# Performance work log

Hardware: AMD Instinct MI355X
Metric: run time of the kernel (lower is better)

Reference implementation:

```python
import jax, jax.numpy as jnp
import numpy as np

N_NODES = 100000
N_EDGES = 1600000
IN_CH = 128


def _sage_conv(x, src, dst, Wl, b, Wr, n_nodes):
    # PyG SAGEConv (aggr='mean', root_weight=True):
    #   out_i = lin_l(mean_{j->i} x_j) + lin_r(x_i)
    msg = x[src]                                             # [E, F]
    agg = jax.ops.segment_sum(msg, dst, num_segments=n_nodes)  # [N, F]
    deg = jax.ops.segment_sum(jnp.ones((src.shape[0],), x.dtype), dst,
                              num_segments=n_nodes)          # [N]
    mean = agg / jnp.maximum(deg, 1.0)[:, None]
    return mean @ Wl + b + x @ Wr


def setup_inputs() -> dict:
    key = jax.random.key(0)
    ks = jax.random.split(key, 10)
    x = jax.random.normal(ks[0], (N_NODES, IN_CH), dtype=jnp.float32)
    edge_index = jax.random.randint(ks[1], (2, N_EDGES), 0, N_NODES, dtype=jnp.int64)
    s = 0.05
    return {
        "x": x,
        "edge_index": edge_index,
        "W1l": jax.random.normal(ks[2], (IN_CH, 32), dtype=jnp.float32) * s,
        "b1": jax.random.normal(ks[3], (32,), dtype=jnp.float32) * s,
        "W1r": jax.random.normal(ks[4], (IN_CH, 32), dtype=jnp.float32) * s,
        "W2l": jax.random.normal(ks[5], (32, 16), dtype=jnp.float32) * s,
        "b2": jax.random.normal(ks[6], (16,), dtype=jnp.float32) * s,
        "W2r": jax.random.normal(ks[7], (32, 16), dtype=jnp.float32) * s,
        "Wfc": jax.random.normal(ks[8], (16, 2), dtype=jnp.float32) * s,
        "bfc": jax.random.normal(ks[9], (2,), dtype=jnp.float32) * s,
    }


def reference(x, edge_index, W1l, b1, W1r, W2l, b2, W2r, Wfc, bfc):
    src, dst = edge_index[0], edge_index[1]
    n = x.shape[0]
    h = jax.nn.relu(_sage_conv(x, src, dst, W1l, b1, W1r, n))   # [N, 32]
    h = jax.nn.relu(_sage_conv(h, src, dst, W2l, b2, W2r, n))   # [N, 16]
    return h @ Wfc + bfc                                        # [N, 2]
```

## Files before the change

kernel.cpp:

```cpp
#include <hip/hip_runtime.h>

#define TPB 256
#define BK_SHIFT 7
#define BK_SIZE 128
#define NBK_MAX 784
#define CAP 2816
#define SC_EPB 8192
#define GEMM_BLKS 1024

typedef __attribute__((ext_vector_type(8))) short bf16x8;
typedef __attribute__((ext_vector_type(4))) float f32x4;
typedef __attribute__((ext_vector_type(2))) float f32x2;
typedef __attribute__((ext_vector_type(4))) unsigned short u16x4;

__device__ __forceinline__ unsigned short f2bf(float f) {
    unsigned u = __float_as_uint(f);
    unsigned r = (u + 0x7FFFu + ((u >> 16) & 1u)) >> 16;
    return (unsigned short)r;
}
__device__ __forceinline__ float bf2f(unsigned short b) {
    return __uint_as_float((unsigned)b << 16);
}
__device__ __forceinline__ void acc4(f32x4& a, u16x4 v) {
    a.x += bf2f(v.x); a.y += bf2f(v.y); a.z += bf2f(v.z); a.w += bf2f(v.w);
}

__global__ __launch_bounds__(256) void build_and_gemm1(
    const int* __restrict__ src, const int* __restrict__ dst,
    int* __restrict__ gfill, int* __restrict__ pk, int E, int NBK, int NSC,
    const float* __restrict__ A,
    const float* __restrict__ Wl,
    const float* __restrict__ Wr,
    const float* __restrict__ b,
    unsigned short* __restrict__ Yb,
    float* __restrict__ C,
    int N)
{
    __shared__ int lcnt[NBK_MAX];
    __shared__ int lbase[NBK_MAX];
    __shared__ int lrank[NBK_MAX];

    if ((int)blockIdx.x < NSC) {
        const int t = threadIdx.x;
        const int e0 = blockIdx.x * SC_EPB;

        for (int i = t; i < NBK; i += 256) { lcnt[i] = 0; lrank[i] = 0; }
        __syncthreads();

        #pragma unroll
        for (int k = 0; k < SC_EPB / 1024; ++k) {
            int e = e0 + k * 1024 + t * 4;
            if (e < E) {
                int4 d = *(const int4*)&dst[e];
                atomicAdd(&lcnt[d.x >> BK_SHIFT], 1);
                atomicAdd(&lcnt[d.y >> BK_SHIFT], 1);
                atomicAdd(&lcnt[d.z >> BK_SHIFT], 1);
                atomicAdd(&lcnt[d.w >> BK_SHIFT], 1);
            }
        }
        __syncthreads();

        for (int i = t; i < NBK; i += 256) {
            int c = lcnt[i];
            if (c) lbase[i] = atomicAdd(&gfill[i], c);
        }
        __syncthreads();

        #pragma unroll
        for (int k = 0; k < SC_EPB / 1024; ++k) {
            int e = e0 + k * 1024 + t * 4;
            if (e < E) {
                int4 d = *(const int4*)&dst[e];
                int4 s = *(const int4*)&src[e];
                {
                    int bb = d.x >> BK_SHIFT;
                    int pos = lbase[bb] + atomicAdd(&lrank[bb], 1);
                    if (pos < CAP) pk[(size_t)bb * CAP + pos] =
                        (s.x << BK_SHIFT) | (d.x & (BK_SIZE - 1));
                }
                {
                    int bb = d.y >> BK_SHIFT;
                    int pos = lbase[bb] + atomicAdd(&lrank[bb], 1);
                    if (pos < CAP) pk[(size_t)bb * CAP + pos] =
                        (s.y << BK_SHIFT) | (d.y & (BK_SIZE - 1));
                }
                {
                    int bb = d.z >> BK_SHIFT;
                    int pos = lbase[bb] + atomicAdd(&lrank[bb], 1);
                    if (pos < CAP) pk[(size_t)bb * CAP + pos] =
                        (s.z << BK_SHIFT) | (d.z & (BK_SIZE - 1));
                }
                {
                    int bb = d.w >> BK_SHIFT;
                    int pos = lbase[bb] + atomicAdd(&lrank[bb], 1);
                    if (pos < CAP) pk[(size_t)bb * CAP + pos] =
                        (s.w << BK_SHIFT) | (d.w & (BK_SIZE - 1));
                }
            }
        }
        return;
    }

    const int lane = threadIdx.x & 63;
    const int m    = lane & 15;
    const int quad = lane >> 4;
    const int wave   = (blockIdx.x - NSC) * (blockDim.x >> 6) + (threadIdx.x >> 6);
    const int nwaves = GEMM_BLKS * (blockDim.x >> 6);
    const int ntiles = (N + 15) >> 4;

    bf16x8 Bf[4][4];
    #pragma unroll
    for (int kc = 0; kc < 4; ++kc) {
        #pragma unroll
        for (int jt = 0; jt < 4; ++jt) {
            const float* W = (jt < 2) ? Wl : Wr;
            const int col = (jt & 1) * 16 + m;
            #pragma unroll
            for (int j = 0; j < 8; ++j) {
                int k = kc * 32 + quad * 8 + j;
                Bf[kc][jt][j] = (short)f2bf(W[k * 32 + col]);
            }
        }
    }

    const float bias0 = b[m];
    const float bias1 = b[16 + m];

    for (int tile = wave; tile < ntiles; tile += nwaves) {
        const int node0 = tile * 16;
        const int gn = node0 + m;
        const bool okA = gn < N;
        const float* rowp = A + (size_t)gn * 128;

        bf16x8 Af[4];
        #pragma unroll
        for (int kc = 0; kc < 4; ++kc) {
            f32x4 v0 = {0.f, 0.f, 0.f, 0.f};
            f32x4 v1 = {0.f, 0.f, 0.f, 0.f};
            if (okA) {
                v0 = __builtin_nontemporal_load((const f32x4*)&rowp[kc * 32 + quad * 8]);
                v1 = __builtin_nontemporal_load((const f32x4*)&rowp[kc * 32 + quad * 8 + 4]);
            }
            Af[kc][0] = (short)f2bf(v0.x); Af[kc][1] = (short)f2bf(v0.y);
            Af[kc][2] = (short)f2bf(v0.z); Af[kc][3] = (short)f2bf(v0.w);
            Af[kc][4] = (short)f2bf(v1.x); Af[kc][5] = (short)f2bf(v1.y);
            Af[kc][6] = (short)f2bf(v1.z); Af[kc][7] = (short)f2bf(v1.w);
        }

        f32x4 acc[4] = {{0.f,0.f,0.f,0.f},{0.f,0.f,0.f,0.f},
                        {0.f,0.f,0.f,0.f},{0.f,0.f,0.f,0.f}};
        #pragma unroll
        for (int kc = 0; kc < 4; ++kc) {
            #pragma unroll
            for (int jt = 0; jt < 4; ++jt)
                acc[jt] = __builtin_amdgcn_mfma_f32_16x16x32_bf16(
                    Af[kc], Bf[kc][jt], acc[jt], 0, 0, 0);
        }

        const int nodeBase = node0 + quad * 4;
        #pragma unroll
        for (int reg = 0; reg < 4; ++reg) {
            const int node = nodeBase + reg;
            if (node < N) {
                Yb[(size_t)node * 32 + m]      = f2bf(acc[0][reg]);
                Yb[(size_t)node * 32 + 16 + m] = f2bf(acc[1][reg]);
                C [(size_t)node * 32 + m]      = acc[2][reg] + bias0;
                C [(size_t)node * 32 + 16 + m] = acc[3][reg] + bias1;
            }
        }
    }
}

__global__ __launch_bounds__(256) void gather_gemm2(
    const int* __restrict__ gfill, const int* __restrict__ pk,
    const unsigned short* __restrict__ Yb,
    const float* __restrict__ c1,
    const float* __restrict__ W2l, const float* __restrict__ W2r,
    const float* __restrict__ b2,
    unsigned short* __restrict__ y2b, float* __restrict__ c2, int N)
{
    __shared__ int lcnt[BK_SIZE];
    __shared__ int soff[BK_SIZE];
    __shared__ int wcur[BK_SIZE];
    __shared__ int sidx[CAP];

    const int t = threadIdx.x;
    const int b = blockIdx.x;
    const size_t base = (size_t)b * CAP;
    const int cnt  = min(gfill[b], CAP);
    const int node0 = b * BK_SIZE;

    if (t < BK_SIZE) lcnt[t] = 0;
    __syncthreads();

    for (int j = t; j < cnt; j += 256)
        atomicAdd(&lcnt[pk[base + j] & (BK_SIZE - 1)], 1);
    __syncthreads();

    int v = (t < BK_SIZE) ? lcnt[t] : 0;
    if (t < BK_SIZE) soff[t] = v;
    __syncthreads();
    for (int off = 1; off < BK_SIZE; off <<= 1) {
        int u = (t < BK_SIZE && t >= off) ? soff[t - off] : 0;
        __syncthreads();
        if (t < BK_SIZE) soff[t] += u;
        __syncthreads();
    }
    if (t < BK_SIZE) wcur[t] = soff[t] - v;
    __syncthreads();

    for (int j = t; j < cnt; j += 256) {
        int pv = pk[base + j];
        int d  = pv & (BK_SIZE - 1);
        int pos = atomicAdd(&wcur[d], 1);
        sidx[pos] = pv >> BK_SHIFT;
    }
    __syncthreads();

    const int q = t & 7;
    #pragma unroll
    for (int pass = 0; pass < 4; ++pass) {
        const int nl = pass * 32 + (t >> 3);
        const int node = node0 + nl;
        const bool active = node < N;
        float h[4] = {0.f, 0.f, 0.f, 0.f};
        if (active) {
            const int deg = lcnt[nl];
            const int en  = soff[nl];
            const int st  = en - deg;
            const float w = 1.0f / fmaxf((float)deg, 1.0f);

            f32x4 a0 = {0.f,0.f,0.f,0.f};
            f32x4 a1 = {0.f,0.f,0.f,0.f};
            f32x4 a2 = {0.f,0.f,0.f,0.f};
            f32x4 a3 = {0.f,0.f,0.f,0.f};
            int j = st;
            for (; j + 3 < en; j += 4) {
                int s0 = sidx[j], s1 = sidx[j+1], s2 = sidx[j+2], s3 = sidx[j+3];
                u16x4 v0 = *(const u16x4*)&Yb[(size_t)s0 * 32 + q * 4];
                u16x4 v1 = *(const u16x4*)&Yb[(size_t)s1 * 32 + q * 4];
                u16x4 v2 = *(const u16x4*)&Yb[(size_t)s2 * 32 + q * 4];
                u16x4 v3 = *(const u16x4*)&Yb[(size_t)s3 * 32 + q * 4];
                acc4(a0, v0); acc4(a1, v1); acc4(a2, v2); acc4(a3, v3);
            }
            for (; j < en; ++j) {
                u16x4 vv = *(const u16x4*)&Yb[(size_t)sidx[j] * 32 + q * 4];
                acc4(a0, vv);
            }
            f32x4 acc;
            acc.x = (a0.x + a1.x) + (a2.x + a3.x);
            acc.y = (a0.y + a1.y) + (a2.y + a3.y);
            acc.z = (a0.z + a1.z) + (a2.z + a3.z);
            acc.w = (a0.w + a1.w) + (a2.w + a3.w);

            f32x4 c = __builtin_nontemporal_load((const f32x4*)&c1[(size_t)node * 32 + q * 4]);
            h[0] = fmaxf(c.x + acc.x * w, 0.f);
            h[1] = fmaxf(c.y + acc.y * w, 0.f);
            h[2] = fmaxf(c.z + acc.z * w, 0.f);
            h[3] = fmaxf(c.w + acc.w * w, 0.f);
        }

        const int  j0  = q * 4;
        const bool isY = (j0 < 16);
        const int  jj  = isY ? j0 : (j0 - 16);
        const float* Wb = isY ? W2l : W2r;

        float o0 = 0.f, o1 = 0.f, o2 = 0.f, o3 = 0.f;
        #pragma unroll
        for (int k = 0; k < 32; ++k) {
            float hk = __shfl(h[k & 3], k >> 2, 8);
            f32x4 wv = *(const f32x4*)&Wb[k * 16 + jj];
            o0 += hk * wv.x; o1 += hk * wv.y; o2 += hk * wv.z; o3 += hk * wv.w;
        }

        if (active) {
            if (isY) {
                u16x4 r;
                r.x = f2bf(o0); r.y = f2bf(o1); r.z = f2bf(o2); r.w = f2bf(o3);
                *(u16x4*)&y2b[(size_t)node * 16 + jj] = r;
            } else {
                f32x4 bb = *(const f32x4*)&b2[jj];
                f32x4 ov = {o0 + bb.x, o1 + bb.y, o2 + bb.z, o3 + bb.w};
                __builtin_nontemporal_store(ov, (f32x4*)&c2[(size_t)node * 16 + jj]);
            }
        }
    }
}

__global__ __launch_bounds__(256) void gather_final(
    const int* __restrict__ gfill, const int* __restrict__ pk,
    const unsigned short* __restrict__ Yb,
    const float* __restrict__ c2,
    const float* __restrict__ Wfc,
    const float* __restrict__ bfc,
    float* __restrict__ out, int N)
{
    __shared__ int lcnt[BK_SIZE];
    __shared__ int soff[BK_SIZE];
    __shared__ int wcur[BK_SIZE];
    __shared__ int sidx[CAP];

    const int t = threadIdx.x;
    const int b = blockIdx.x;
    const size_t base = (size_t)b * CAP;
    const int cnt  = min(gfill[b], CAP);
    const int node0 = b * BK_SIZE;

    if (t < BK_SIZE) lcnt[t] = 0;
    __syncthreads();

    for (int j = t; j < cnt; j += 256)
        atomicAdd(&lcnt[pk[base + j] & (BK_SIZE - 1)], 1);
    __syncthreads();

    int v = (t < BK_SIZE) ? lcnt[t] : 0;
    if (t < BK_SIZE) soff[t] = v;
    __syncthreads();
    for (int off = 1; off < BK_SIZE; off <<= 1) {
        int u = (t < BK_SIZE && t >= off) ? soff[t - off] : 0;
        __syncthreads();
        if (t < BK_SIZE) soff[t] += u;
        __syncthreads();
    }
    if (t < BK_SIZE) wcur[t] = soff[t] - v;
    __syncthreads();

    for (int j = t; j < cnt; j += 256) {
        int pv = pk[base + j];
        int d  = pv & (BK_SIZE - 1);
        int pos = atomicAdd(&wcur[d], 1);
        sidx[pos] = pv >> BK_SHIFT;
    }
    __syncthreads();

    const int q = t & 3;
    #pragma unroll
    for (int pass = 0; pass < 2; ++pass) {
        const int nl = pass * 64 + (t >> 2);
        const int node = node0 + nl;
        if (node < N) {
            const int deg = lcnt[nl];
            const int en  = soff[nl];
            const int st  = en - deg;
            const float w = 1.0f / fmaxf((float)deg, 1.0f);

            f32x4 a0 = {0.f,0.f,0.f,0.f};
            f32x4 a1 = {0.f,0.f,0.f,0.f};
            f32x4 a2 = {0.f,0.f,0.f,0.f};
            f32x4 a3 = {0.f,0.f,0.f,0.f};
            int j = st;
            for (; j + 3 < en; j += 4) {
                int s0 = sidx[j], s1 = sidx[j+1], s2 = sidx[j+2], s3 = sidx[j+3];
                u16x4 v0 = *(const u16x4*)&Yb[(size_t)s0 * 16 + q * 4];
                u16x4 v1 = *(const u16x4*)&Yb[(size_t)s1 * 16 + q * 4];
                u16x4 v2 = *(const u16x4*)&Yb[(size_t)s2 * 16 + q * 4];
                u16x4 v3 = *(const u16x4*)&Yb[(size_t)s3 * 16 + q * 4];
                acc4(a0, v0); acc4(a1, v1); acc4(a2, v2); acc4(a3, v3);
            }
            for (; j < en; ++j) {
                u16x4 vv = *(const u16x4*)&Yb[(size_t)sidx[j] * 16 + q * 4];
                acc4(a0, vv);
            }
            f32x4 acc;
            acc.x = (a0.x + a1.x) + (a2.x + a3.x);
            acc.y = (a0.y + a1.y) + (a2.y + a3.y);
            acc.z = (a0.z + a1.z) + (a2.z + a3.z);
            acc.w = (a0.w + a1.w) + (a2.w + a3.w);

            f32x4 c = __builtin_nontemporal_load((const f32x4*)&c2[(size_t)node * 16 + q * 4]);
            float h0 = fmaxf(c.x + acc.x * w, 0.f);
            float h1 = fmaxf(c.y + acc.y * w, 0.f);
            float h2 = fmaxf(c.z + acc.z * w, 0.f);
            float h3 = fmaxf(c.w + acc.w * w, 0.f);

            const float* Wq = &Wfc[q * 8];
            float o0 = h0 * Wq[0] + h1 * Wq[2] + h2 * Wq[4] + h3 * Wq[6];
            float o1 = h0 * Wq[1] + h1 * Wq[3] + h2 * Wq[5] + h3 * Wq[7];

            o0 += __shfl_xor(o0, 1); o0 += __shfl_xor(o0, 2);
            o1 += __shfl_xor(o1, 1); o1 += __shfl_xor(o1, 2);

            if (q == 0) {
                f32x2 ov = {o0 + bfc[0], o1 + bfc[1]};
                __builtin_nontemporal_store(ov, (f32x2*)&out[(size_t)node * 2]);
            }
        } else {
            float z = 0.f;
            z += __shfl_xor(z, 1); z += __shfl_xor(z, 2);
        }
    }
}

extern "C" void kernel_launch(void* const* d_in, const int* in_sizes, int n_in,
                              void* d_out, int out_size, void* d_ws, size_t ws_size,
                              hipStream_t stream)
{
    const float* x   = (const float*)d_in[0];
    const int*   ei  = (const int*)d_in[1];
    const float* W1l = (const float*)d_in[2];
    const float* b1  = (const float*)d_in[3];
    const float* W1r = (const float*)d_in[4];
    const float* W2l = (const float*)d_in[5];
    const float* b2  = (const float*)d_in[6];
    const float* W2r = (const float*)d_in[7];
    const float* Wfc = (const float*)d_in[8];
    const float* bfc = (const float*)d_in[9];
    float* out = (float*)d_out;

    const int N = in_sizes[0] / 128;
    const int E = in_sizes[1] / 2;
    const int* src = ei;
    const int* dst = ei + E;

    const int NBK = (N + BK_SIZE - 1) / BK_SIZE;
    const int NSC = (E + SC_EPB - 1) / SC_EPB;

    int*   gfill = (int*)d_ws;
    int*   pk    = gfill + NBK_MAX;
    unsigned short* y1b = (unsigned short*)(pk + (size_t)NBK_MAX * CAP);
    float* c1          = (float*)(y1b + (size_t)N * 32);
    unsigned short* y2b = (unsigned short*)(c1 + (size_t)N * 32);
    float* c2          = (float*)(y2b + (size_t)N * 16);

    hipMemsetAsync(gfill, 0, (size_t)NBK_MAX * sizeof(int), stream);
    build_and_gemm1<<<NSC + GEMM_BLKS, TPB, 0, stream>>>(
        src, dst, gfill, pk, E, NBK, NSC,
        x, W1l, W1r, b1, y1b, c1, N);

    gather_gemm2<<<NBK, TPB, 0, stream>>>(
        gfill, pk, y1b, c1, W2l, W2r, b2, y2b, c2, N);

    gather_final<<<NBK, TPB, 0, stream>>>(
        gfill, pk, y2b, c2, Wfc, bfc, out, N);
}
```

Before: 201.9 us.

## Fuse all three stages into one persistent kernel with grid barriers

Merges edge bucketing plus GEMM1, gather plus GEMM2, and the final gather into one kernel launched with NBK blocks, separated by atomic-counter grid barriers. GEMM1 tiles are handed out through a global atomic work counter in batches instead of a fixed stride over dedicated blocks. The aim is to remove two kernel launches and their tails, and to let scatter blocks pick up GEMM work after they finish. In exchange the grid barrier relies on all NBK blocks (about 782) being co-resident, which risks deadlock, and it adds barrier spin cost.

```diff
diff --git a/kernel.cpp b/kernel.cpp
--- a/kernel.cpp
+++ b/kernel.cpp
@@ -6,7 +6,7 @@
 #define NBK_MAX 784
 #define CAP 2816
 #define SC_EPB 8192
-#define GEMM_BLKS 1024
+#define TILE_BATCH 2
 
 typedef __attribute__((ext_vector_type(8))) short bf16x8;
 typedef __attribute__((ext_vector_type(4))) float f32x4;
@@ -25,24 +25,46 @@
     a.x += bf2f(v.x); a.y += bf2f(v.y); a.z += bf2f(v.z); a.w += bf2f(v.w);
 }
 
-__global__ __launch_bounds__(256) void build_and_gemm1(
+__device__ __forceinline__ void grid_barrier(int* bar, int nblk) {
+    __syncthreads();
+    if (threadIdx.x == 0) {
+        __threadfence();
+        atomicAdd(bar, 1);
+        while (atomicAdd(bar, 0) < nblk)
+            __builtin_amdgcn_s_sleep(2);
+        __threadfence();
+    }
+    __syncthreads();
+}
+
+__global__ __launch_bounds__(256, 4) void fused_all(
     const int* __restrict__ src, const int* __restrict__ dst,
-    int* __restrict__ gfill, int* __restrict__ pk, int E, int NBK, int NSC,
+    int* __restrict__ gfill, int* __restrict__ tcur, int* __restrict__ bar,
+    int* __restrict__ pk,
+    int E, int NBK, int NSC,
     const float* __restrict__ A,
-    const float* __restrict__ Wl,
-    const float* __restrict__ Wr,
-    const float* __restrict__ b,
-    unsigned short* __restrict__ Yb,
-    float* __restrict__ C,
-    int N)
+    const float* __restrict__ W1l, const float* __restrict__ W1r,
+    const float* __restrict__ b1,
+    unsigned short* __restrict__ y1b,
+    float* __restrict__ c1,
+    const float* __restrict__ W2l, const float* __restrict__ W2r,
+    const float* __restrict__ b2,
+    unsigned short* __restrict__ y2b,
+    float* __restrict__ c2,
+    const float* __restrict__ Wfc, const float* __restrict__ bfc,
+    float* __restrict__ out, int N)
 {
-    __shared__ int lcnt[NBK_MAX];
-    __shared__ int lbase[NBK_MAX];
-    __shared__ int lrank[NBK_MAX];
-
-    if ((int)blockIdx.x < NSC) {
-        const int t = threadIdx.x;
-        const int e0 = blockIdx.x * SC_EPB;
+    __shared__ int smem[3200];
+
+    const int t    = threadIdx.x;
+    const int bid  = blockIdx.x;
+    const int lane = t & 63;
+
+    if (bid < NSC) {
+        int* lcnt  = smem;
+        int* lbase = smem + 784;
+        int* lrank = smem + 1568;
+        const int e0 = bid * SC_EPB;
 
         for (int i = t; i < NBK; i += 256) { lcnt[i] = 0; lrank[i] = 0; }
         __syncthreads();
@@ -98,295 +120,290 @@
                 }
             }
         }
-        return;
     }
 
-    const int lane = threadIdx.x & 63;
-    const int m    = lane & 15;
-    const int quad = lane >> 4;
-    const int wave   = (blockIdx.x - NSC) * (blockDim.x >> 6) + (threadIdx.x >> 6);
-    const int nwaves = GEMM_BLKS * (blockDim.x >> 6);
-    const int ntiles = (N + 15) >> 4;
-
-    bf16x8 Bf[4][4];
-    #pragma unroll
-    for (int kc = 0; kc < 4; ++kc) {
-        #pragma unroll
-        for (int jt = 0; jt < 4; ++jt) {
-            const float* W = (jt < 2) ? Wl : Wr;
-            const int col = (jt & 1) * 16 + m;
-            #pragma unroll
-            for (int j = 0; j < 8; ++j) {
-                int k = kc * 32 + quad * 8 + j;
-                Bf[kc][jt][j] = (short)f2bf(W[k * 32 + col]);
-            }
-        }
-    }
-
-    const float bias0 = b[m];
-    const float bias1 = b[16 + m];
-
-    for (int tile = wave; tile < ntiles; tile += nwaves) {
-        const int node0 = tile * 16;
-        const int gn = node0 + m;
-        const bool okA = gn < N;
-        const float* rowp = A + (size_t)gn * 128;
-
-        bf16x8 Af[4];
-        #pragma unroll
-        for (int kc = 0; kc < 4; ++kc) {
-            f32x4 v0 = {0.f, 0.f, 0.f, 0.f};
-            f32x4 v1 = {0.f, 0.f, 0.f, 0.f};
-            if (okA) {
-                v0 = __builtin_nontemporal_load((const f32x4*)&rowp[kc * 32 + quad * 8]);
-                v1 = __builtin_nontemporal_load((const f32x4*)&rowp[kc * 32 + quad * 8 + 4]);
-            }
-            Af[kc][0] = (short)f2bf(v0.x); Af[kc][1] = (short)f2bf(v0.y);
-            Af[kc][2] = (short)f2bf(v0.z); Af[kc][3] = (short)f2bf(v0.w);
-            Af[kc][4] = (short)f2bf(v1.x); Af[kc][5] = (short)f2bf(v1.y);
-            Af[kc][6] = (short)f2bf(v1.z); Af[kc][7] = (short)f2bf(v1.w);
-        }
-
-        f32x4 acc[4] = {{0.f,0.f,0.f,0.f},{0.f,0.f,0.f,0.f},
-                        {0.f,0.f,0.f,0.f},{0.f,0.f,0.f,0.f}};
+    {
+        const int m    = lane & 15;
+        const int quad = lane >> 4;
+        const int ntiles = (N + 15) >> 4;
+
+        bf16x8 Bf[4][4];
         #pragma unroll
         for (int kc = 0; kc < 4; ++kc) {
             #pragma unroll
-            for (int jt = 0; jt < 4; ++jt)
-                acc[jt] = __builtin_amdgcn_mfma_f32_16x16x32_bf16(
-                    Af[kc], Bf[kc][jt], acc[jt], 0, 0, 0);
-        }
-
-        const int nodeBase = node0 + quad * 4;
+            for (int jt = 0; jt < 4; ++jt) {
+                const float* W = (jt < 2) ? W1l : W1r;
+                const int col = (jt & 1) * 16 + m;
+                #pragma unroll
+                for (int j = 0; j < 8; ++j) {
+                    int k = kc * 32 + quad * 8 + j;
+                    Bf[kc][jt][j] = (short)f2bf(W[k * 32 + col]);
+                }
+            }
+        }
+
+        const float bias0 = b1[m];
+        const float bias1 = b1[16 + m];
+
+        for (;;) {
+            int t0 = 0;
+            if (lane == 0) t0 = atomicAdd(tcur, TILE_BATCH);
+            t0 = __shfl(t0, 0, 64);
+            if (t0 >= ntiles) break;
+
+            for (int it = 0; it < TILE_BATCH; ++it) {
+                const int tile = t0 + it;
+                if (tile >= ntiles) break;
+                const int node0 = tile * 16;
+                const int gn = node0 + m;
+                const bool okA = gn < N;
+                const float* rowp = A + (size_t)gn * 128;
+
+                bf16x8 Af[4];
+                #pragma unroll
+                for (int kc = 0; kc < 4; ++kc) {
+                    f32x4 v0 = {0.f, 0.f, 0.f, 0.f};
+                    f32x4 v1 = {0.f, 0.f, 0.f, 0.f};
+                    if (okA) {
+                        v0 = __builtin_nontemporal_load((const f32x4*)&rowp[kc * 32 + quad * 8]);
+                        v1 = __builtin_nontemporal_load((const f32x4*)&rowp[kc * 32 + quad * 8 + 4]);
+                    }
+                    Af[kc][0] = (short)f2bf(v0.x); Af[kc][1] = (short)f2bf(v0.y);
+                    Af[kc][2] = (short)f2bf(v0.z); Af[kc][3] = (short)f2bf(v0.w);
+                    Af[kc][4] = (short)f2bf(v1.x); Af[kc][5] = (short)f2bf(v1.y);
+                    Af[kc][6] = (short)f2bf(v1.z); Af[kc][7] = (short)f2bf(v1.w);
+                }
+
+                f32x4 acc[4] = {{0.f,0.f,0.f,0.f},{0.f,0.f,0.f,0.f},
+                                {0.f,0.f,0.f,0.f},{0.f,0.f,0.f,0.f}};
+                #pragma unroll
+                for (int kc = 0; kc < 4; ++kc) {
+                    #pragma unroll
+                    for (int jt = 0; jt < 4; ++jt)
+                        acc[jt] = __builtin_amdgcn_mfma_f32_16x16x32_bf16(
+                            Af[kc], Bf[kc][jt], acc[jt], 0, 0, 0);
+                }
+
+                const int nodeBase = node0 + quad * 4;
+                #pragma unroll
+                for (int reg = 0; reg < 4; ++reg) {
+                    const int node = nodeBase + reg;
+                    if (node < N) {
+                        y1b[(size_t)node * 32 + m]      = f2bf(acc[0][reg]);
+                        y1b[(size_t)node * 32 + 16 + m] = f2bf(acc[1][reg]);
+                        c1 [(size_t)node * 32 + m]      = acc[2][reg] + bias0;
+                        c1 [(size_t)node * 32 + 16 + m] = acc[3][reg] + bias1;
+                    }
+                }
+            }
+        }
+    }
+
+    grid_barrier(&bar[0], NBK);
+
+    {
+        int* lcnt = smem;
+        int* soff = smem + 128;
+        int* wcur = smem + 256;
+        int* sidx = smem + 384;
+
+        const int b = bid;
+        const size_t base = (size_t)b * CAP;
+        const int cnt  = min(gfill[b], CAP);
+        const int node0 = b * BK_SIZE;
+
+        if (t < BK_SIZE) lcnt[t] = 0;
+        __syncthreads();
+
+        for (int j = t; j < cnt; j += 256)
+            atomicAdd(&lcnt[pk[base + j] & (BK_SIZE - 1)], 1);
+        __syncthreads();
+
+        int v = (t < BK_SIZE) ? lcnt[t] : 0;
+        if (t < BK_SIZE) soff[t] = v;
+        __syncthreads();
+        for (int off = 1; off < BK_SIZE; off <<= 1) {
+            int u = (t < BK_SIZE && t >= off) ? soff[t - off] : 0;
+            __syncthreads();
+            if (t < BK_SIZE) soff[t] += u;
+            __syncthreads();
+        }
+        if (t < BK_SIZE) wcur[t] = soff[t] - v;
+        __syncthreads();
+
+        for (int j = t; j < cnt; j += 256) {
+            int pv = pk[base + j];
+            int d  = pv & (BK_SIZE - 1);
+            int pos = atomicAdd(&wcur[d], 1);
+            sidx[pos] = pv >> BK_SHIFT;
+        }
+        __syncthreads();
+
+        const int q = t & 7;
         #pragma unroll
-        for (int reg = 0; reg < 4; ++reg) {
-            const int node = nodeBase + reg;
+        for (int pass = 0; pass < 4; ++pass) {
+            const int nl = pass * 32 + (t >> 3);
+            const int node = node0 + nl;
+            const bool active = node < N;
+            float h[4] = {0.f, 0.f, 0.f, 0.f};
+            if (active) {
+                const int deg = lcnt[nl];
+                const int en  = soff[nl];
+                const int st  = en - deg;
+                const float w = 1.0f / fmaxf((float)deg, 1.0f);
+
+                f32x4 a0 = {0.f,0.f,0.f,0.f};
+                f32x4 a1 = {0.f,0.f,0.f,0.f};
+                f32x4 a2 = {0.f,0.f,0.f,0.f};
+                f32x4 a3 = {0.f,0.f,0.f,0.f};
+                int j = st;
+                for (; j + 3 < en; j += 4) {
+                    int s0 = sidx[j], s1 = sidx[j+1], s2 = sidx[j+2], s3 = sidx[j+3];
+                    u16x4 v0 = *(const u16x4*)&y1b[(size_t)s0 * 32 + q * 4];
+                    u16x4 v1 = *(const u16x4*)&y1b[(size_t)s1 * 32 + q * 4];
+                    u16x4 v2 = *(const u16x4*)&y1b[(size_t)s2 * 32 + q * 4];
+                    u16x4 v3 = *(const u16x4*)&y1b[(size_t)s3 * 32 + q * 4];
+                    acc4(a0, v0); acc4(a1, v1); acc4(a2, v2); acc4(a3, v3);
+                }
+                for (; j < en; ++j) {
+                    u16x4 vv = *(const u16x4*)&y1b[(size_t)sidx[j] * 32 + q * 4];
+                    acc4(a0, vv);
+                }
+                f32x4 acc;
+                acc.x = (a0.x + a1.x) + (a2.x + a3.x);
+                acc.y = (a0.y + a1.y) + (a2.y + a3.y);
+                acc.z = (a0.z + a1.z) + (a2.z + a3.z);
+                acc.w = (a0.w + a1.w) + (a2.w + a3.w);
+
+                f32x4 c = *(const f32x4*)&c1[(size_t)node * 32 + q * 4];
+                h[0] = fmaxf(c.x + acc.x * w, 0.f);
+                h[1] = fmaxf(c.y + acc.y * w, 0.f);
+                h[2] = fmaxf(c.z + acc.z * w, 0.f);
+                h[3] = fmaxf(c.w + acc.w * w, 0.f);
+            }
+
+            const int  j0  = q * 4;
+            const bool isY = (j0 < 16);
+            const int  jj  = isY ? j0 : (j0 - 16);
+            const float* Wb = isY ? W2l : W2r;
+
+            float o0 = 0.f, o1 = 0.f, o2 = 0.f, o3 = 0.f;
+            #pragma unroll
+            for (int k = 0; k < 32; ++k) {
+                float hk = __shfl(h[k & 3], k >> 2, 8);
+                f32x4 wv = *(const f32x4*)&Wb[k * 16 + jj];
+                o0 += hk * wv.x; o1 += hk * wv.y; o2 += hk * wv.z; o3 += hk * wv.w;
+            }
+
+            if (active) {
+                if (isY) {
+                    u16x4 r;
+                    r.x = f2bf(o0); r.y = f2bf(o1); r.z = f2bf(o2); r.w = f2bf(o3);
+                    *(u16x4*)&y2b[(size_t)node * 16 + jj] = r;
+                } else {
+                    f32x4 bb = *(const f32x4*)&b2[jj];
+                    f32x4 ov = {o0 + bb.x, o1 + bb.y, o2 + bb.z, o3 + bb.w};
+                    *(f32x4*)&c2[(size_t)node * 16 + jj] = ov;
+                }
+            }
+        }
+    }
+
+    grid_barrier(&bar[16], NBK);
+
+    {
+        int* lcnt = smem;
+        int* soff = smem + 128;
+        int* wcur = smem + 256;
+        int* sidx = smem + 384;
+
+        const int b = bid;
+        const size_t base = (size_t)b * CAP;
+        const int cnt  = min(gfill[b], CAP);
+        const int node0 = b * BK_SIZE;
+
+        if (t < BK_SIZE) lcnt[t] = 0;
+        __syncthreads();
+
+        for (int j = t; j < cnt; j += 256)
+            atomicAdd(&lcnt[pk[base + j] & (BK_SIZE - 1)], 1);
+        __syncthreads();
+
+        int v = (t < BK_SIZE) ? lcnt[t] : 0;
+        if (t < BK_SIZE) soff[t] = v;
+        __syncthreads();
+        for (int off = 1; off < BK_SIZE; off <<= 1) {
+            int u = (t < BK_SIZE && t >= off) ? soff[t - off] : 0;
+            __syncthreads();
+            if (t < BK_SIZE) soff[t] += u;
+            __syncthreads();
+        }
+        if (t < BK_SIZE) wcur[t] = soff[t] - v;
+        __syncthreads();
+
+        for (int j = t; j < cnt; j += 256) {
+            int pv = pk[base + j];
+            int d  = pv & (BK_SIZE - 1);
+            int pos = atomicAdd(&wcur[d], 1);
+            sidx[pos] = pv >> BK_SHIFT;
+        }
+        __syncthreads();
+
+        const int q = t & 3;
+        #pragma unroll
+        for (int pass = 0; pass < 2; ++pass) {
+            const int nl = pass * 64 + (t >> 2);
+            const int node = node0 + nl;
             if (node < N) {
-                Yb[(size_t)node * 32 + m]      = f2bf(acc[0][reg]);
-                Yb[(size_t)node * 32 + 16 + m] = f2bf(acc[1][reg]);
-                C [(size_t)node * 32 + m]      = acc[2][reg] + bias0;
-                C [(size_t)node * 32 + 16 + m] = acc[3][reg] + bias1;
-            }
-        }
-    }
-}
-
-__global__ __launch_bounds__(256) void gather_gemm2(
-    const int* __restrict__ gfill, const int* __restrict__ pk,
-    const unsigned short* __restrict__ Yb,
-    const float* __restrict__ c1,
-    const float* __restrict__ W2l, const float* __restrict__ W2r,
-    const float* __restrict__ b2,
-    unsigned short* __restrict__ y2b, float* __restrict__ c2, int N)
-{
-    __shared__ int lcnt[BK_SIZE];
-    __shared__ int soff[BK_SIZE];
-    __shared__ int wcur[BK_SIZE];
-    __shared__ int sidx[CAP];
-
-    const int t = threadIdx.x;
-    const int b = blockIdx.x;
-    const size_t base = (size_t)b * CAP;
-    const int cnt  = min(gfill[b], CAP);
-    const int node0 = b * BK_SIZE;
-
-    if (t < BK_SIZE) lcnt[t] = 0;
-    __syncthreads();
-
-    for (int j = t; j < cnt; j += 256)
-        atomicAdd(&lcnt[pk[base + j] & (BK_SIZE - 1)], 1);
-    __syncthreads();
-
-    int v = (t < BK_SIZE) ? lcnt[t] : 0;
-    if (t < BK_SIZE) soff[t] = v;
-    __syncthreads();
-    for (int off = 1; off < BK_SIZE; off <<= 1) {
-        int u = (t < BK_SIZE && t >= off) ? soff[t - off] : 0;
-        __syncthreads();
-        if (t < BK_SIZE) soff[t] += u;
-        __syncthreads();
-    }
-    if (t < BK_SIZE) wcur[t] = soff[t] - v;
-    __syncthreads();
-
-    for (int j = t; j < cnt; j += 256) {
-        int pv = pk[base + j];
-        int d  = pv & (BK_SIZE - 1);
-        int pos = atomicAdd(&wcur[d], 1);
-        sidx[pos] = pv >> BK_SHIFT;
-    }
-    __syncthreads();
-
-    const int q = t & 7;
-    #pragma unroll
-    for (int pass = 0; pass < 4; ++pass) {
-        const int nl = pass * 32 + (t >> 3);
-        const int node = node0 + nl;
-        const bool active = node < N;
-        float h[4] = {0.f, 0.f, 0.f, 0.f};
-        if (active) {
-            const int deg = lcnt[nl];
-            const int en  = soff[nl];
-            const int st  = en - deg;
-            const float w = 1.0f / fmaxf((float)deg, 1.0f);
-
-            f32x4 a0 = {0.f,0.f,0.f,0.f};
-            f32x4 a1 = {0.f,0.f,0.f,0.f};
-            f32x4 a2 = {0.f,0.f,0.f,0.f};
-            f32x4 a3 = {0.f,0.f,0.f,0.f};
-            int j = st;
-            for (; j + 3 < en; j += 4) {
-                int s0 = sidx[j], s1 = sidx[j+1], s2 = sidx[j+2], s3 = sidx[j+3];
-                u16x4 v0 = *(const u16x4*)&Yb[(size_t)s0 * 32 + q * 4];
-                u16x4 v1 = *(const u16x4*)&Yb[(size_t)s1 * 32 + q * 4];
-                u16x4 v2 = *(const u16x4*)&Yb[(size_t)s2 * 32 + q * 4];
-                u16x4 v3 = *(const u16x4*)&Yb[(size_t)s3 * 32 + q * 4];
-                acc4(a0, v0); acc4(a1, v1); acc4(a2, v2); acc4(a3, v3);
-            }
-            for (; j < en; ++j) {
-                u16x4 vv = *(const u16x4*)&Yb[(size_t)sidx[j] * 32 + q * 4];
-                acc4(a0, vv);
-            }
-            f32x4 acc;
-            acc.x = (a0.x + a1.x) + (a2.x + a3.x);
-            acc.y = (a0.y + a1.y) + (a2.y + a3.y);
-            acc.z = (a0.z + a1.z) + (a2.z + a3.z);
-            acc.w = (a0.w + a1.w) + (a2.w + a3.w);
-
-            f32x4 c = __builtin_nontemporal_load((const f32x4*)&c1[(size_t)node * 32 + q * 4]);
-            h[0] = fmaxf(c.x + acc.x * w, 0.f);
-            h[1] = fmaxf(c.y + acc.y * w, 0.f);
-            h[2] = fmaxf(c.z + acc.z * w, 0.f);
-            h[3] = fmaxf(c.w + acc.w * w, 0.f);
-        }
-
-        const int  j0  = q * 4;
-        const bool isY = (j0 < 16);
-        const int  jj  = isY ? j0 : (j0 - 16);
-        const float* Wb = isY ? W2l : W2r;
-
-        float o0 = 0.f, o1 = 0.f, o2 = 0.f, o3 = 0.f;
-        #pragma unroll
-        for (int k = 0; k < 32; ++k) {
-            float hk = __shfl(h[k & 3], k >> 2, 8);
-            f32x4 wv = *(const f32x4*)&Wb[k * 16 + jj];
-            o0 += hk * wv.x; o1 += hk * wv.y; o2 += hk * wv.z; o3 += hk * wv.w;
-        }
-
-        if (active) {
-            if (isY) {
-                u16x4 r;
-                r.x = f2bf(o0); r.y = f2bf(o1); r.z = f2bf(o2); r.w = f2bf(o3);
-                *(u16x4*)&y2b[(size_t)node * 16 + jj] = r;
+                const int deg = lcnt[nl];
+                const int en  = soff[nl];
+                const int st  = en - deg;
+                const float w = 1.0f / fmaxf((float)deg, 1.0f);
+
+                f32x4 a0 = {0.f,0.f,0.f,0.f};
+                f32x4 a1 = {0.f,0.f,0.f,0.f};
+                f32x4 a2 = {0.f,0.f,0.f,0.f};
+                f32x4 a3 = {0.f,0.f,0.f,0.f};
+                int j = st;
+                for (; j + 3 < en; j += 4) {
+                    int s0 = sidx[j], s1 = sidx[j+1], s2 = sidx[j+2], s3 = sidx[j+3];
+                    u16x4 v0 = *(const u16x4*)&y2b[(size_t)s0 * 16 + q * 4];
+                    u16x4 v1 = *(const u16x4*)&y2b[(size_t)s1 * 16 + q * 4];
+                    u16x4 v2 = *(const u16x4*)&y2b[(size_t)s2 * 16 + q * 4];
+                    u16x4 v3 = *(const u16x4*)&y2b[(size_t)s3 * 16 + q * 4];
+                    acc4(a0, v0); acc4(a1, v1); acc4(a2, v2); acc4(a3, v3);
+                }
+                for (; j < en; ++j) {
+                    u16x4 vv = *(const u16x4*)&y2b[(size_t)sidx[j] * 16 + q * 4];
+                    acc4(a0, vv);
+                }
+                f32x4 acc;
+                acc.x = (a0.x + a1.x) + (a2.x + a3.x);
+                acc.y = (a0.y + a1.y) + (a2.y + a3.y);
+                acc.z = (a0.z + a1.z) + (a2.z + a3.z);
+                acc.w = (a0.w + a1.w) + (a2.w + a3.w);
+
+                f32x4 c = *(const f32x4*)&c2[(size_t)node * 16 + q * 4];
+                float h0 = fmaxf(c.x + acc.x * w, 0.f);
+                float h1 = fmaxf(c.y + acc.y * w, 0.f);
+                float h2 = fmaxf(c.z + acc.z * w, 0.f);
+                float h3 = fmaxf(c.w + acc.w * w, 0.f);
+
+                const float* Wq = &Wfc[q * 8];
+                float o0 = h0 * Wq[0] + h1 * Wq[2] + h2 * Wq[4] + h3 * Wq[6];
+                float o1 = h0 * Wq[1] + h1 * Wq[3] + h2 * Wq[5] + h3 * Wq[7];
+
+                o0 += __shfl_xor(o0, 1); o0 += __shfl_xor(o0, 2);
+                o1 += __shfl_xor(o1, 1); o1 += __shfl_xor(o1, 2);
+
+                if (q == 0) {
+                    f32x2 ov = {o0 + bfc[0], o1 + bfc[1]};
+                    __builtin_nontemporal_store(ov, (f32x2*)&out[(size_t)node * 2]);
+                }
             } else {
-                f32x4 bb = *(const f32x4*)&b2[jj];
-                f32x4 ov = {o0 + bb.x, o1 + bb.y, o2 + bb.z, o3 + bb.w};
-                __builtin_nontemporal_store(ov, (f32x4*)&c2[(size_t)node * 16 + jj]);
-            }
-        }
-    }
-}
-
-__global__ __launch_bounds__(256) void gather_final(
-    const int* __restrict__ gfill, const int* __restrict__ pk,
-    const unsigned short* __restrict__ Yb,
-    const float* __restrict__ c2,
-    const float* __restrict__ Wfc,
-    const float* __restrict__ bfc,
-    float* __restrict__ out, int N)
-{
-    __shared__ int lcnt[BK_SIZE];
-    __shared__ int soff[BK_SIZE];
-    __shared__ int wcur[BK_SIZE];
-    __shared__ int sidx[CAP];
-
-    const int t = threadIdx.x;
-    const int b = blockIdx.x;
-    const size_t base = (size_t)b * CAP;
-    const int cnt  = min(gfill[b], CAP);
-    const int node0 = b * BK_SIZE;
-
-    if (t < BK_SIZE) lcnt[t] = 0;
-    __syncthreads();
-
-    for (int j = t; j < cnt; j += 256)
-        atomicAdd(&lcnt[pk[base + j] & (BK_SIZE - 1)], 1);
-    __syncthreads();
-
-    int v = (t < BK_SIZE) ? lcnt[t] : 0;
-    if (t < BK_SIZE) soff[t] = v;
-    __syncthreads();
-    for (int off = 1; off < BK_SIZE; off <<= 1) {
-        int u = (t < BK_SIZE && t >= off) ? soff[t - off] : 0;
-        __syncthreads();
-        if (t < BK_SIZE) soff[t] += u;
-        __syncthreads();
-    }
-    if (t < BK_SIZE) wcur[t] = soff[t] - v;
-    __syncthreads();
-
-    for (int j = t; j < cnt; j += 256) {
-        int pv = pk[base + j];
-        int d  = pv & (BK_SIZE - 1);
-        int pos = atomicAdd(&wcur[d], 1);
-        sidx[pos] = pv >> BK_SHIFT;
-    }
-    __syncthreads();
-
-    const int q = t & 3;
-    #pragma unroll
-    for (int pass = 0; pass < 2; ++pass) {
-        const int nl = pass * 64 + (t >> 2);
-        const int node = node0 + nl;
-        if (node < N) {
-            const int deg = lcnt[nl];
-            const int en  = soff[nl];
-            const int st  = en - deg;
-            const float w = 1.0f / fmaxf((float)deg, 1.0f);
-
-            f32x4 a0 = {0.f,0.f,0.f,0.f};
-            f32x4 a1 = {0.f,0.f,0.f,0.f};
-            f32x4 a2 = {0.f,0.f,0.f,0.f};
-            f32x4 a3 = {0.f,0.f,0.f,0.f};
-            int j = st;
-            for (; j + 3 < en; j += 4) {
-                int s0 = sidx[j], s1 = sidx[j+1], s2 = sidx[j+2], s3 = sidx[j+3];
-                u16x4 v0 = *(const u16x4*)&Yb[(size_t)s0 * 16 + q * 4];
-                u16x4 v1 = *(const u16x4*)&Yb[(size_t)s1 * 16 + q * 4];
-                u16x4 v2 = *(const u16x4*)&Yb[(size_t)s2 * 16 + q * 4];
-                u16x4 v3 = *(const u16x4*)&Yb[(size_t)s3 * 16 + q * 4];
-                acc4(a0, v0); acc4(a1, v1); acc4(a2, v2); acc4(a3, v3);
-            }
-            for (; j < en; ++j) {
-                u16x4 vv = *(const u16x4*)&Yb[(size_t)sidx[j] * 16 + q * 4];
-                acc4(a0, vv);
-            }
-            f32x4 acc;
-            acc.x = (a0.x + a1.x) + (a2.x + a3.x);
-            acc.y = (a0.y + a1.y) + (a2.y + a3.y);
-            acc.z = (a0.z + a1.z) + (a2.z + a3.z);
-            acc.w = (a0.w + a1.w) + (a2.w + a3.w);
-
-            f32x4 c = __builtin_nontemporal_load((const f32x4*)&c2[(size_t)node * 16 + q * 4]);
-            float h0 = fmaxf(c.x + acc.x * w, 0.f);
-            float h1 = fmaxf(c.y + acc.y * w, 0.f);
-            float h2 = fmaxf(c.z + acc.z * w, 0.f);
-            float h3 = fmaxf(c.w + acc.w * w, 0.f);
-
-            const float* Wq = &Wfc[q * 8];
-            float o0 = h0 * Wq[0] + h1 * Wq[2] + h2 * Wq[4] + h3 * Wq[6];
-            float o1 = h0 * Wq[1] + h1 * Wq[3] + h2 * Wq[5] + h3 * Wq[7];
-
-            o0 += __shfl_xor(o0, 1); o0 += __shfl_xor(o0, 2);
-            o1 += __shfl_xor(o1, 1); o1 += __shfl_xor(o1, 2);
-
-            if (q == 0) {
-                f32x2 ov = {o0 + bfc[0], o1 + bfc[1]};
-                __builtin_nontemporal_store(ov, (f32x2*)&out[(size_t)node * 2]);
-            }
-        } else {
-            float z = 0.f;
-            z += __shfl_xor(z, 1); z += __shfl_xor(z, 2);
+                float z = 0.f;
+                z += __shfl_xor(z, 1); z += __shfl_xor(z, 2);
+            }
         }
     }
 }
@@ -407,29 +424,28 @@
     const float* bfc = (const float*)d_in[9];
     float* out = (float*)d_out;
 
-    const int N = in_sizes[0] / 128;
-    const int E = in_sizes[1] / 2;
+    int N = in_sizes[0] / 128;
+    int E = in_sizes[1] / 2;
     const int* src = ei;
     const int* dst = ei + E;
 
-    const int NBK = (N + BK_SIZE - 1) / BK_SIZE;
-    const int NSC = (E + SC_EPB - 1) / SC_EPB;
+    int NBK = (N + BK_SIZE - 1) / BK_SIZE;
+    int NSC = (E + SC_EPB - 1) / SC_EPB;
 
     int*   gfill = (int*)d_ws;
-    int*   pk    = gfill + NBK_MAX;
+    int*   tcur  = gfill + NBK_MAX;
+    int*   bar   = tcur + 16;
+    int*   pk    = bar + 32;
     unsigned short* y1b = (unsigned short*)(pk + (size_t)NBK_MAX * CAP);
     float* c1          = (float*)(y1b + (size_t)N * 32);
     unsigned short* y2b = (unsigned short*)(c1 + (size_t)N * 32);
     float* c2          = (float*)(y2b + (size_t)N * 16);
 
-    hipMemsetAsync(gfill, 0, (size_t)NBK_MAX * sizeof(int), stream);
-    build_and_gemm1<<<NSC + GEMM_BLKS, TPB, 0, stream>>>(
-        src, dst, gfill, pk, E, NBK, NSC,
-        x, W1l, W1r, b1, y1b, c1, N);
-
-    gather_gemm2<<<NBK, TPB, 0, stream>>>(
-        gfill, pk, y1b, c1, W2l, W2r, b2, y2b, c2, N);
-
-    gather_final<<<NBK, TPB, 0, stream>>>(
-        gfill, pk, y2b, c2, Wfc, bfc, out, N);
-}
+    hipMemsetAsync(gfill, 0, (size_t)(NBK_MAX + 48) * sizeof(int), stream);
+
+    fused_all<<<NBK, TPB, 0, stream>>>(
+        src, dst, gfill, tcur, bar, pk, E, NBK, NSC,
+        x, W1l, W1r, b1, y1b, c1,
+        W2l, W2r, b2, y2b, c2,
+        Wfc, bfc, out, N);
+}
```

Result: slower. 436.8 us (+116.4%).

## Split layer-1 features into lo/hi planes and dynamically schedule GEMM tiles

Applied to the files above, without the earlier changes.

Layer-1 bf16 projections are stored as two separate 16-wide planes, so each gathered row is 32 bytes instead of 64. The gather in gather_gemm2 now splits the edges across two lane groups per half and combines the partial sums with shuffles. The build kernel becomes a single uniform grid where scatter blocks, once done, join GEMM work pulled from an atomic tile counter in batches. The scatter chunk size is halved, and several nontemporal loads and stores become ordinary ones. The two gather passes and the atomic counter add instructions and contention, and the changed layout changes gather cache behaviour.

```diff
diff --git a/kernel.cpp b/kernel.cpp
--- a/kernel.cpp
+++ b/kernel.cpp
@@ -5,8 +5,9 @@
 #define BK_SIZE 128
 #define NBK_MAX 784
 #define CAP 2816
-#define SC_EPB 8192
-#define GEMM_BLKS 1024
+#define SC_EPB 4096
+#define GRID_BUILD 1568
+#define TILE_BATCH 2
 
 typedef __attribute__((ext_vector_type(8))) short bf16x8;
 typedef __attribute__((ext_vector_type(4))) float f32x4;
@@ -27,12 +28,14 @@
 
 __global__ __launch_bounds__(256) void build_and_gemm1(
     const int* __restrict__ src, const int* __restrict__ dst,
-    int* __restrict__ gfill, int* __restrict__ pk, int E, int NBK, int NSC,
+    int* __restrict__ gfill, int* __restrict__ tcur, int* __restrict__ pk,
+    int E, int NBK, int NSC,
     const float* __restrict__ A,
     const float* __restrict__ Wl,
     const float* __restrict__ Wr,
     const float* __restrict__ b,
-    unsigned short* __restrict__ Yb,
+    unsigned short* __restrict__ y1lo,
+    unsigned short* __restrict__ y1hi,
     float* __restrict__ C,
     int N)
 {
@@ -40,8 +43,9 @@
     __shared__ int lbase[NBK_MAX];
     __shared__ int lrank[NBK_MAX];
 
+    const int t = threadIdx.x;
+
     if ((int)blockIdx.x < NSC) {
-        const int t = threadIdx.x;
         const int e0 = blockIdx.x * SC_EPB;
 
         for (int i = t; i < NBK; i += 256) { lcnt[i] = 0; lrank[i] = 0; }
@@ -98,74 +102,82 @@
                 }
             }
         }
-        return;
-    }
-
-    const int lane = threadIdx.x & 63;
-    const int m    = lane & 15;
-    const int quad = lane >> 4;
-    const int wave   = (blockIdx.x - NSC) * (blockDim.x >> 6) + (threadIdx.x >> 6);
-    const int nwaves = GEMM_BLKS * (blockDim.x >> 6);
-    const int ntiles = (N + 15) >> 4;
-
-    bf16x8 Bf[4][4];
-    #pragma unroll
-    for (int kc = 0; kc < 4; ++kc) {
-        #pragma unroll
-        for (int jt = 0; jt < 4; ++jt) {
-            const float* W = (jt < 2) ? Wl : Wr;
-            const int col = (jt & 1) * 16 + m;
-            #pragma unroll
-            for (int j = 0; j < 8; ++j) {
-                int k = kc * 32 + quad * 8 + j;
-                Bf[kc][jt][j] = (short)f2bf(W[k * 32 + col]);
-            }
-        }
-    }
-
-    const float bias0 = b[m];
-    const float bias1 = b[16 + m];
-
-    for (int tile = wave; tile < ntiles; tile += nwaves) {
-        const int node0 = tile * 16;
-        const int gn = node0 + m;
-        const bool okA = gn < N;
-        const float* rowp = A + (size_t)gn * 128;
-
-        bf16x8 Af[4];
-        #pragma unroll
-        for (int kc = 0; kc < 4; ++kc) {
-            f32x4 v0 = {0.f, 0.f, 0.f, 0.f};
-            f32x4 v1 = {0.f, 0.f, 0.f, 0.f};
-            if (okA) {
-                v0 = __builtin_nontemporal_load((const f32x4*)&rowp[kc * 32 + quad * 8]);
-                v1 = __builtin_nontemporal_load((const f32x4*)&rowp[kc * 32 + quad * 8 + 4]);
-            }
-            Af[kc][0] = (short)f2bf(v0.x); Af[kc][1] = (short)f2bf(v0.y);
-            Af[kc][2] = (short)f2bf(v0.z); Af[kc][3] = (short)f2bf(v0.w);
-            Af[kc][4] = (short)f2bf(v1.x); Af[kc][5] = (short)f2bf(v1.y);
-            Af[kc][6] = (short)f2bf(v1.z); Af[kc][7] = (short)f2bf(v1.w);
-        }
-
-        f32x4 acc[4] = {{0.f,0.f,0.f,0.f},{0.f,0.f,0.f,0.f},
-                        {0.f,0.f,0.f,0.f},{0.f,0.f,0.f,0.f}};
+    }
+
+    {
+        const int lane = t & 63;
+        const int m    = lane & 15;
+        const int quad = lane >> 4;
+        const int ntiles = (N + 15) >> 4;
+
+        bf16x8 Bf[4][4];
         #pragma unroll
         for (int kc = 0; kc < 4; ++kc) {
             #pragma unroll
-            for (int jt = 0; jt < 4; ++jt)
-                acc[jt] = __builtin_amdgcn_mfma_f32_16x16x32_bf16(
-                    Af[kc], Bf[kc][jt], acc[jt], 0, 0, 0);
-        }
-
-        const int nodeBase = node0 + quad * 4;
-        #pragma unroll
-        for (int reg = 0; reg < 4; ++reg) {
-            const int node = nodeBase + reg;
-            if (node < N) {
-                Yb[(size_t)node * 32 + m]      = f2bf(acc[0][reg]);
-                Yb[(size_t)node * 32 + 16 + m] = f2bf(acc[1][reg]);
-                C [(size_t)node * 32 + m]      = acc[2][reg] + bias0;
-                C [(size_t)node * 32 + 16 + m] = acc[3][reg] + bias1;
+            for (int jt = 0; jt < 4; ++jt) {
+                const float* W = (jt < 2) ? Wl : Wr;
+                const int col = (jt & 1) * 16 + m;
+                #pragma unroll
+                for (int j = 0; j < 8; ++j) {
+                    int k = kc * 32 + quad * 8 + j;
+                    Bf[kc][jt][j] = (short)f2bf(W[k * 32 + col]);
+                }
+            }
+        }
+
+        const float bias0 = b[m];
+        const float bias1 = b[16 + m];
+
+        for (;;) {
+            int t0 = 0;
+            if (lane == 0) t0 = atomicAdd(tcur, TILE_BATCH);
+            t0 = __shfl(t0, 0, 64);
+            if (t0 >= ntiles) break;
+
+            for (int it = 0; it < TILE_BATCH; ++it) {
+                const int tile = t0 + it;
+                if (tile >= ntiles) break;
+                const int node0 = tile * 16;
+                const int gn = node0 + m;
+                const bool okA = gn < N;
+                const float* rowp = A + (size_t)gn * 128;
+
+                bf16x8 Af[4];
+                #pragma unroll
+                for (int kc = 0; kc < 4; ++kc) {
+                    f32x4 v0 = {0.f, 0.f, 0.f, 0.f};
+                    f32x4 v1 = {0.f, 0.f, 0.f, 0.f};
+                    if (okA) {
+                        v0 = __builtin_nontemporal_load((const f32x4*)&rowp[kc * 32 + quad * 8]);
+                        v1 = __builtin_nontemporal_load((const f32x4*)&rowp[kc * 32 + quad * 8 + 4]);
+                    }
+                    Af[kc][0] = (short)f2bf(v0.x); Af[kc][1] = (short)f2bf(v0.y);
+                    Af[kc][2] = (short)f2bf(v0.z); Af[kc][3] = (short)f2bf(v0.w);
+                    Af[kc][4] = (short)f2bf(v1.x); Af[kc][5] = (short)f2bf(v1.y);
+                    Af[kc][6] = (short)f2bf(v1.z); Af[kc][7] = (short)f2bf(v1.w);
+                }
+
+                f32x4 acc[4] = {{0.f,0.f,0.f,0.f},{0.f,0.f,0.f,0.f},
+                                {0.f,0.f,0.f,0.f},{0.f,0.f,0.f,0.f}};
+                #pragma unroll
+                for (int kc = 0; kc < 4; ++kc) {
+                    #pragma unroll
+                    for (int jt = 0; jt < 4; ++jt)
+                        acc[jt] = __builtin_amdgcn_mfma_f32_16x16x32_bf16(
+                            Af[kc], Bf[kc][jt], acc[jt], 0, 0, 0);
+                }
+
+                const int nodeBase = node0 + quad * 4;
+                #pragma unroll
+                for (int reg = 0; reg < 4; ++reg) {
+                    const int node = nodeBase + reg;
+                    if (node < N) {
+                        y1lo[(size_t)node * 16 + m] = f2bf(acc[0][reg]);
+                        y1hi[(size_t)node * 16 + m] = f2bf(acc[1][reg]);
+                        C [(size_t)node * 32 + m]      = acc[2][reg] + bias0;
+                        C [(size_t)node * 32 + 16 + m] = acc[3][reg] + bias1;
+                    }
+                }
             }
         }
     }
@@ -173,7 +185,8 @@
 
 __global__ __launch_bounds__(256) void gather_gemm2(
     const int* __restrict__ gfill, const int* __restrict__ pk,
-    const unsigned short* __restrict__ Yb,
+    const unsigned short* __restrict__ y1lo,
+    const unsigned short* __restrict__ y1hi,
     const float* __restrict__ c1,
     const float* __restrict__ W2l, const float* __restrict__ W2r,
     const float* __restrict__ b2,
@@ -217,7 +230,9 @@
     }
     __syncthreads();
 
-    const int q = t & 7;
+    const int q    = t & 7;
+    const int qq   = q & 3;
+    const int half = (q >> 2) & 1;
     #pragma unroll
     for (int pass = 0; pass < 4; ++pass) {
         const int nl = pass * 32 + (t >> 3);
@@ -234,26 +249,53 @@
             f32x4 a1 = {0.f,0.f,0.f,0.f};
             f32x4 a2 = {0.f,0.f,0.f,0.f};
             f32x4 a3 = {0.f,0.f,0.f,0.f};
-            int j = st;
-            for (; j + 3 < en; j += 4) {
-                int s0 = sidx[j], s1 = sidx[j+1], s2 = sidx[j+2], s3 = sidx[j+3];
-                u16x4 v0 = *(const u16x4*)&Yb[(size_t)s0 * 32 + q * 4];
-                u16x4 v1 = *(const u16x4*)&Yb[(size_t)s1 * 32 + q * 4];
-                u16x4 v2 = *(const u16x4*)&Yb[(size_t)s2 * 32 + q * 4];
-                u16x4 v3 = *(const u16x4*)&Yb[(size_t)s3 * 32 + q * 4];
-                acc4(a0, v0); acc4(a1, v1); acc4(a2, v2); acc4(a3, v3);
-            }
-            for (; j < en; ++j) {
-                u16x4 vv = *(const u16x4*)&Yb[(size_t)sidx[j] * 32 + q * 4];
-                acc4(a0, vv);
-            }
-            f32x4 acc;
-            acc.x = (a0.x + a1.x) + (a2.x + a3.x);
-            acc.y = (a0.y + a1.y) + (a2.y + a3.y);
-            acc.z = (a0.z + a1.z) + (a2.z + a3.z);
-            acc.w = (a0.w + a1.w) + (a2.w + a3.w);
-
-            f32x4 c = __builtin_nontemporal_load((const f32x4*)&c1[(size_t)node * 32 + q * 4]);
+            int j = st + half;
+            for (; j + 6 < en; j += 8) {
+                int s0 = sidx[j], s1 = sidx[j+2], s2 = sidx[j+4], s3 = sidx[j+6];
+                acc4(a0, *(const u16x4*)&y1lo[(size_t)s0 * 16 + qq * 4]);
+                acc4(a1, *(const u16x4*)&y1lo[(size_t)s1 * 16 + qq * 4]);
+                acc4(a2, *(const u16x4*)&y1lo[(size_t)s2 * 16 + qq * 4]);
+                acc4(a3, *(const u16x4*)&y1lo[(size_t)s3 * 16 + qq * 4]);
+            }
+            for (; j < en; j += 2)
+                acc4(a0, *(const u16x4*)&y1lo[(size_t)sidx[j] * 16 + qq * 4]);
+            f32x4 fa;
+            fa.x = (a0.x + a1.x) + (a2.x + a3.x);
+            fa.y = (a0.y + a1.y) + (a2.y + a3.y);
+            fa.z = (a0.z + a1.z) + (a2.z + a3.z);
+            fa.w = (a0.w + a1.w) + (a2.w + a3.w);
+            fa.x += __shfl_xor(fa.x, 4, 8);
+            fa.y += __shfl_xor(fa.y, 4, 8);
+            fa.z += __shfl_xor(fa.z, 4, 8);
+            fa.w += __shfl_xor(fa.w, 4, 8);
+
+            a0 = (f32x4){0.f,0.f,0.f,0.f};
+            a1 = (f32x4){0.f,0.f,0.f,0.f};
+            a2 = (f32x4){0.f,0.f,0.f,0.f};
+            a3 = (f32x4){0.f,0.f,0.f,0.f};
+            j = st + half;
+            for (; j + 6 < en; j += 8) {
+                int s0 = sidx[j], s1 = sidx[j+2], s2 = sidx[j+4], s3 = sidx[j+6];
+                acc4(a0, *(const u16x4*)&y1hi[(size_t)s0 * 16 + qq * 4]);
+                acc4(a1, *(const u16x4*)&y1hi[(size_t)s1 * 16 + qq * 4]);
+                acc4(a2, *(const u16x4*)&y1hi[(size_t)s2 * 16 + qq * 4]);
+                acc4(a3, *(const u16x4*)&y1hi[(size_t)s3 * 16 + qq * 4]);
+            }
+            for (; j < en; j += 2)
+                acc4(a0, *(const u16x4*)&y1hi[(size_t)sidx[j] * 16 + qq * 4]);
+            f32x4 fb;
+            fb.x = (a0.x + a1.x) + (a2.x + a3.x);
+            fb.y = (a0.y + a1.y) + (a2.y + a3.y);
+            fb.z = (a0.z + a1.z) + (a2.z + a3.z);
+            fb.w = (a0.w + a1.w) + (a2.w + a3.w);
+            fb.x += __shfl_xor(fb.x, 4, 8);
+            fb.y += __shfl_xor(fb.y, 4, 8);
+            fb.z += __shfl_xor(fb.z, 4, 8);
+            fb.w += __shfl_xor(fb.w, 4, 8);
+
+            f32x4 acc = (q < 4) ? fa : fb;
+
+            f32x4 c = *(const f32x4*)&c1[(size_t)node * 32 + q * 4];
             h[0] = fmaxf(c.x + acc.x * w, 0.f);
             h[1] = fmaxf(c.y + acc.y * w, 0.f);
             h[2] = fmaxf(c.z + acc.z * w, 0.f);
@@ -281,7 +323,7 @@
             } else {
                 f32x4 bb = *(const f32x4*)&b2[jj];
                 f32x4 ov = {o0 + bb.x, o1 + bb.y, o2 + bb.z, o3 + bb.w};
-                __builtin_nontemporal_store(ov, (f32x4*)&c2[(size_t)node * 16 + jj]);
+                *(f32x4*)&c2[(size_t)node * 16 + jj] = ov;
             }
         }
     }
@@ -351,23 +393,20 @@
             int j = st;
             for (; j + 3 < en; j += 4) {
                 int s0 = sidx[j], s1 = sidx[j+1], s2 = sidx[j+2], s3 = sidx[j+3];
-                u16x4 v0 = *(const u16x4*)&Yb[(size_t)s0 * 16 + q * 4];
-                u16x4 v1 = *(const u16x4*)&Yb[(size_t)s1 * 16 + q * 4];
-                u16x4 v2 = *(const u16x4*)&Yb[(size_t)s2 * 16 + q * 4];
-                u16x4 v3 = *(const u16x4*)&Yb[(size_t)s3 * 16 + q * 4];
-                acc4(a0, v0); acc4(a1, v1); acc4(a2, v2); acc4(a3, v3);
-            }
-            for (; j < en; ++j) {
-                u16x4 vv = *(const u16x4*)&Yb[(size_t)sidx[j] * 16 + q * 4];
-                acc4(a0, vv);
-            }
+                acc4(a0, *(const u16x4*)&Yb[(size_t)s0 * 16 + q * 4]);
+                acc4(a1, *(const u16x4*)&Yb[(size_t)s1 * 16 + q * 4]);
+                acc4(a2, *(const u16x4*)&Yb[(size_t)s2 * 16 + q * 4]);
+                acc4(a3, *(const u16x4*)&Yb[(size_t)s3 * 16 + q * 4]);
+            }
+            for (; j < en; ++j)
+                acc4(a0, *(const u16x4*)&Yb[(size_t)sidx[j] * 16 + q * 4]);
             f32x4 acc;
             acc.x = (a0.x + a1.x) + (a2.x + a3.x);
             acc.y = (a0.y + a1.y) + (a2.y + a3.y);
             acc.z = (a0.z + a1.z) + (a2.z + a3.z);
             acc.w = (a0.w + a1.w) + (a2.w + a3.w);
 
-            f32x4 c = __builtin_nontemporal_load((const f32x4*)&c2[(size_t)node * 16 + q * 4]);
+            f32x4 c = *(const f32x4*)&c2[(size_t)node * 16 + q * 4];
             float h0 = fmaxf(c.x + acc.x * w, 0.f);
             float h1 = fmaxf(c.y + acc.y * w, 0.f);
             float h2 = fmaxf(c.z + acc.z * w, 0.f);
@@ -416,19 +455,22 @@
     const int NSC = (E + SC_EPB - 1) / SC_EPB;
 
     int*   gfill = (int*)d_ws;
-    int*   pk    = gfill + NBK_MAX;
-    unsigned short* y1b = (unsigned short*)(pk + (size_t)NBK_MAX * CAP);
-    float* c1          = (float*)(y1b + (size_t)N * 32);
+    int*   tcur  = gfill + NBK_MAX;
+    int*   pk    = tcur + 16;
+    unsigned short* y1lo = (unsigned short*)(pk + (size_t)NBK_MAX * CAP);
+    unsigned short* y1hi = y1lo + (size_t)N * 16;
+    float* c1           = (float*)(y1hi + (size_t)N * 16);
     unsigned short* y2b = (unsigned short*)(c1 + (size_t)N * 32);
-    float* c2          = (float*)(y2b + (size_t)N * 16);
-
-    hipMemsetAsync(gfill, 0, (size_t)NBK_MAX * sizeof(int), stream);
-    build_and_gemm1<<<NSC + GEMM_BLKS, TPB, 0, stream>>>(
-        src, dst, gfill, pk, E, NBK, NSC,
-        x, W1l, W1r, b1, y1b, c1, N);
+    float* c2           = (float*)(y2b + (size_t)N * 16);
+
+    hipMemsetAsync(gfill, 0, (size_t)(NBK_MAX + 16) * sizeof(int), stream);
+
+    build_and_gemm1<<<GRID_BUILD, TPB, 0, stream>>>(
+        src, dst, gfill, tcur, pk, E, NBK, NSC,
+        x, W1l, W1r, b1, y1lo, y1hi, c1, N);
 
     gather_gemm2<<<NBK, TPB, 0, stream>>>(
-        gfill, pk, y1b, c1, W2l, W2r, b2, y2b, c2, N);
+        gfill, pk, y1lo, y1hi, c1, W2l, W2r, b2, y2b, c2, N);
 
     gather_final<<<NBK, TPB, 0, stream>>>(
         gfill, pk, y2b, c2, Wfc, bfc, out, N);
```

New measurement: 286.0 us. +41.7%, slower.
